# Kernel optimization log

Hardware: AMD Instinct MI355X
Metric: run time of the kernel (lower is better)

Reference implementation:

```python
import jax, jax.numpy as jnp
import numpy as np

T, B, E, H = 2048, 4, 768, 12
HD = E // H


def setup_inputs() -> dict:
    root = jax.random.key(0)
    ks = jax.random.split(root, 7)
    def xavier(k, shape):
        fan_in, fan_out = shape[1], shape[0]
        lim = (6.0 / (fan_in + fan_out)) ** 0.5
        return jax.random.uniform(k, shape, jnp.float32, -lim, lim)
    return {
        "query": jax.random.normal(ks[0], (T, B, E), jnp.float32),
        "key": jax.random.normal(ks[1], (T, B, E), jnp.float32),
        "value": jax.random.normal(ks[2], (T, B, E), jnp.float32),
        "in_proj_weight": xavier(ks[3], (3 * E, E)),
        "in_proj_bias": jnp.zeros((3 * E,), jnp.float32),
        "out_w": xavier(ks[4], (E, E)),
        "out_b": jnp.zeros((E,), jnp.float32),
    }


def reference(query, key, value, in_proj_weight, in_proj_bias, out_w, out_b):
    scaling = HD ** -0.5
    # separate Q/K/V projections from slices of the fused in_proj weight
    q = (query @ in_proj_weight[:E].T + in_proj_bias[:E]) * scaling
    k = key @ in_proj_weight[E:2 * E].T + in_proj_bias[E:2 * E]
    v = value @ in_proj_weight[2 * E:].T + in_proj_bias[2 * E:]
    tgt_len, bsz, _ = query.shape
    src_len = key.shape[0]
    # [T,B,E] -> [B,H,T,hd]
    qh = q.reshape(tgt_len, bsz, H, HD).transpose(1, 2, 0, 3)
    kh = k.reshape(src_len, bsz, H, HD).transpose(1, 2, 0, 3)
    vh = v.reshape(src_len, bsz, H, HD).transpose(1, 2, 0, 3)
    # full attention matrix [B,H,T,S] (faithful to the bmm-softmax-bmm impl)
    scores = jnp.einsum("bhqd,bhkd->bhqk", qh, kh)
    weights = jax.nn.softmax(scores, axis=-1)  # attn_dropout = 0.0 (eval)
    attn = jnp.einsum("bhqk,bhkd->bhqd", weights, vh)
    attn = attn.transpose(2, 0, 1, 3).reshape(tgt_len, bsz, E)
    out = attn @ out_w.T + out_b
    avg_weights = weights.sum(axis=1) / H  # [B,T,S]
    return out, avg_weights
```

## Files before the change

### kernel.cpp

```cpp
#include <hip/hip_runtime.h>

typedef unsigned short u16;
typedef unsigned long long u64;
typedef __attribute__((ext_vector_type(8))) short bf16x8;
typedef __attribute__((ext_vector_type(4))) float f32x4;
typedef __attribute__((ext_vector_type(16))) float f32x16;
typedef __attribute__((ext_vector_type(4))) _Float16 f16x4;
typedef __attribute__((ext_vector_type(2))) __fp16 h16x2;

#define TT 2048
#define BB 4
#define EE 768
#define HH 12
#define HD 64
#define NTOK 8192
#define KVB 32
#define NTILE (TT / KVB)

__device__ __forceinline__ u16 f2bf(float f) {
  unsigned int u = __builtin_bit_cast(unsigned int, f);
  u += 0x7fffu + ((u >> 16) & 1u);
  return (u16)(u >> 16);
}

__device__ __forceinline__ float bf2f(u16 b) {
  unsigned int u = (unsigned int)b << 16;
  return __builtin_bit_cast(float, u);
}

__device__ __forceinline__ unsigned int pack2(u16 a, u16 b) {
  return (unsigned int)a | ((unsigned int)b << 16);
}

__device__ __forceinline__ unsigned int cvtpk2(float a, float b) {
  unsigned int r;
  asm("v_cvt_pk_bf16_f32 %0, %1, %2" : "=v"(r) : "v"(a), "v"(b));
  return r;
}

__device__ __forceinline__ unsigned int pkh2(float a, float b) {
  h16x2 t = __builtin_amdgcn_cvt_pkrtz(a, b);
  return __builtin_bit_cast(unsigned int, t);
}

__global__ __launch_bounds__(256, 3) void proj_qkv(
    const float* __restrict__ q_in, const float* __restrict__ k_in, const float* __restrict__ v_in,
    const float* __restrict__ ipw, const float* __restrict__ ipb,
    u16* __restrict__ qh, u16* __restrict__ kh, u16* __restrict__ vh)
{
  __shared__ u16 sA[2][128 * 40];
  __shared__ u16 sB[2][192 * 40];
  const int tid = threadIdx.x;
  const int w = tid >> 6, lane = tid & 63, l32 = lane & 31, hi = lane >> 5;
  const int wm = w & 1, wn = w >> 1;
  const int orig = blockIdx.x;
  const int wg = (orig & 7) * 96 + (orig >> 3);
  const int z = wg >> 8;
  const int rem = wg & 255;
  const int bm = rem >> 2, bn = rem & 3;

  const float* A = (z == 0) ? q_in : (z == 1) ? k_in : v_in;
  const float* W = ipw + (size_t)z * EE * EE;
  const float* bias = ipb + z * EE;

  const int srow = tid >> 3, scs = tid & 7;
  const float* ag = A + (size_t)(bm * 128 + srow) * EE + scs * 4;
  const float* wgp = W + (size_t)(bn * 192 + srow) * EE + scs * 4;

  f32x16 acc[2][3] = {};
  float4 la[4], lw[6];

#pragma unroll
  for (int i = 0; i < 4; ++i) la[i] = *(const float4*)(ag + (size_t)i * 32 * EE);
#pragma unroll
  for (int i = 0; i < 6; ++i) lw[i] = *(const float4*)(wgp + (size_t)i * 32 * EE);
#pragma unroll
  for (int i = 0; i < 4; ++i) {
    u64 pk = (u64)cvtpk2(la[i].x, la[i].y) | ((u64)cvtpk2(la[i].z, la[i].w) << 32);
    *(u64*)&sA[0][(i * 32 + srow) * 40 + scs * 4] = pk;
  }
#pragma unroll
  for (int i = 0; i < 6; ++i) {
    u64 pk = (u64)cvtpk2(lw[i].x, lw[i].y) | ((u64)cvtpk2(lw[i].z, lw[i].w) << 32);
    *(u64*)&sB[0][(i * 32 + srow) * 40 + scs * 4] = pk;
  }

  for (int kt = 0; kt < EE / 32; ++kt) {
    const int buf = kt & 1;
    const bool more = (kt + 1) < EE / 32;
    if (more) {
      const int ko = (kt + 1) * 32;
#pragma unroll
      for (int i = 0; i < 4; ++i) la[i] = *(const float4*)(ag + (size_t)i * 32 * EE + ko);
#pragma unroll
      for (int i = 0; i < 6; ++i) lw[i] = *(const float4*)(wgp + (size_t)i * 32 * EE + ko);
    }
    __syncthreads();
#pragma unroll
    for (int ks = 0; ks < 2; ++ks) {
      bf16x8 bfr[3];
#pragma unroll
      for (int tn = 0; tn < 3; ++tn)
        bfr[tn] = *(const bf16x8*)&sB[buf][(wn * 96 + tn * 32 + l32) * 40 + ks * 16 + hi * 8];
#pragma unroll
      for (int tm = 0; tm < 2; ++tm) {
        bf16x8 afr = *(const bf16x8*)&sA[buf][(wm * 64 + tm * 32 + l32) * 40 + ks * 16 + hi * 8];
#pragma unroll
        for (int tn = 0; tn < 3; ++tn)
          acc[tm][tn] = __builtin_amdgcn_mfma_f32_32x32x16_bf16(afr, bfr[tn], acc[tm][tn], 0, 0, 0);
      }
    }
    if (more) {
      const int nb = buf ^ 1;
#pragma unroll
      for (int i = 0; i < 4; ++i) {
        u64 pk = (u64)cvtpk2(la[i].x, la[i].y) | ((u64)cvtpk2(la[i].z, la[i].w) << 32);
        *(u64*)&sA[nb][(i * 32 + srow) * 40 + scs * 4] = pk;
      }
#pragma unroll
      for (int i = 0; i < 6; ++i) {
        u64 pk = (u64)cvtpk2(lw[i].x, lw[i].y) | ((u64)cvtpk2(lw[i].z, lw[i].w) << 32);
        *(u64*)&sB[nb][(i * 32 + srow) * 40 + scs * 4] = pk;
      }
    }
  }

  const float scale = (z == 0) ? 0.125f : 1.0f;
  u16* dst = (z == 0) ? qh : (z == 1) ? kh : vh;
#pragma unroll
  for (int tn = 0; tn < 3; ++tn) {
    const int j = bn * 192 + wn * 96 + tn * 32 + l32;
    const int h = j >> 6, d = j & 63;
    const float bj = bias[j];
#pragma unroll
    for (int tm = 0; tm < 2; ++tm) {
#pragma unroll
      for (int r = 0; r < 16; ++r) {
        int m = bm * 128 + wm * 64 + tm * 32 + (r & 3) + 8 * (r >> 2) + 4 * hi;
        int t = m >> 2, bb = m & 3;
        float v = (acc[tm][tn][r] + bj) * scale;
        dst[((size_t)((bb * HH + h) * TT + t)) * HD + d] = f2bf(v);
      }
    }
  }
}

__global__ __launch_bounds__(256) void transpose_v(
    const u16* __restrict__ vh, _Float16* __restrict__ vhT)
{
  __shared__ u16 tile[64][72];
  const int tid = threadIdx.x;
  const int bh = blockIdx.y;
  const int t0 = blockIdx.x * 64;
  {
    int row = tid >> 2, seg = tid & 3;
    const u16* src = vh + (size_t)bh * TT * HD + (size_t)(t0 + row) * HD + seg * 16;
    uint4 a = *(const uint4*)(src);
    uint4 b = *(const uint4*)(src + 8);
    *(uint4*)&tile[row][seg * 16] = a;
    *(uint4*)&tile[row][seg * 16 + 8] = b;
  }
  __syncthreads();
  {
    int d = tid >> 2, ts = tid & 3;
    u16 tmp[16];
#pragma unroll
    for (int i = 0; i < 16; ++i) tmp[i] = tile[ts * 16 + i][d];
    unsigned int pk[8];
#pragma unroll
    for (int i = 0; i < 8; ++i)
      pk[i] = pkh2(bf2f(tmp[2 * i]), bf2f(tmp[2 * i + 1]));
    uint4 o0, o1;
    o0.x = pk[0]; o0.y = pk[1]; o0.z = pk[2]; o0.w = pk[3];
    o1.x = pk[4]; o1.y = pk[5]; o1.z = pk[6]; o1.w = pk[7];
    _Float16* dst = vhT + (size_t)bh * HD * TT + (size_t)d * TT + t0 + ts * 16;
    *(uint4*)dst = o0;
    *(uint4*)(dst + 8) = o1;
  }
}

__global__ __launch_bounds__(256, 3) void attn_flash(
    const u16* __restrict__ qh, const u16* __restrict__ kh, const _Float16* __restrict__ vhT,
    u16* __restrict__ ctx, float* __restrict__ stats_rl)
{
  __shared__ u16 sK[2][KVB * 64];
  __shared__ _Float16 sV[2][64 * 36];

  const int tid = threadIdx.x, w = tid >> 6, lane = tid & 63;
  const int l16 = lane & 15, quad = lane >> 4;
  const int orig = blockIdx.x;
  const int wg = (orig & 7) * 96 + (orig >> 3);
  const int qb = wg & 15;
  const int bhl = wg >> 4;
  const int b = bhl / HH, h = bhl - b * HH;
  const int q0 = qb * 128 + w * 32;
  const size_t bh = (size_t)bhl;
  const u16* qg = qh + (bh * TT + q0) * HD;
  const u16* kg = kh + bh * TT * HD;
  const _Float16* vg = vhT + bh * HD * TT;

  const int krow = tid >> 3, kch = tid & 7;
  const int kdst = krow * 64 + ((kch ^ (krow & 7)) * 8);
  const u16* kgp = kg + (size_t)krow * HD + kch * 8;
  const int vrow = tid >> 2, vch = tid & 3;
  const int vdst = vrow * 36 + vch * 8;
  const _Float16* vgp = vg + (size_t)vrow * TT + vch * 8;

  bf16x8 qf[2][2];
#pragma unroll
  for (int j = 0; j < 2; ++j)
#pragma unroll
    for (int p = 0; p < 2; ++p)
      qf[j][p] = *(const bf16x8*)(qg + (j * 16 + l16) * HD + p * 32 + quad * 8);

  f32x4 oacc[2][4] = {};
  float lsum[2] = {0.0f, 0.0f};

  {
    uint4 kv = *(const uint4*)kgp;
    uint4 vv = *(const uint4*)vgp;
    *(uint4*)&sK[0][kdst] = kv;
    *(u64*)&sV[0][vdst]     = ((const u64*)&vv)[0];
    *(u64*)&sV[0][vdst + 4] = ((const u64*)&vv)[1];
  }

  for (int st = 0; st < NTILE; ++st) {
    const int buf = st & 1;
    uint4 nk, nv;
    const bool more = (st + 1 < NTILE);
    if (more) {
      nk = *(const uint4*)(kgp + (size_t)(st + 1) * KVB * HD);
      nv = *(const uint4*)(vgp + (st + 1) * KVB);
    }
    __syncthreads();

    const u16* kb = &sK[buf][0];
    const _Float16* vb = &sV[buf][0];
#pragma unroll
    for (int ss = 0; ss < 2; ++ss) {
      const int krw = ss * 16 + l16;
      bf16x8 kf0 = *(const bf16x8*)&kb[krw * 64 + ((quad ^ (krw & 7)) * 8)];
      bf16x8 kf1 = *(const bf16x8*)&kb[krw * 64 + (((4 + quad) ^ (krw & 7)) * 8)];
      f16x4 vf[4];
#pragma unroll
      for (int m = 0; m < 4; ++m)
        vf[m] = *(const f16x4*)&vb[(m * 16 + l16) * 36 + ss * 16 + quad * 4];
#pragma unroll
      for (int j = 0; j < 2; ++j) {
        f32x4 z = {};
        f32x4 T = __builtin_amdgcn_mfma_f32_16x16x32_bf16(kf0, qf[j][0], z, 0, 0, 0);
        T = __builtin_amdgcn_mfma_f32_16x16x32_bf16(kf1, qf[j][1], T, 0, 0, 0);
        float p0 = __expf(T[0]), p1 = __expf(T[1]), p2 = __expf(T[2]), p3 = __expf(T[3]);
        lsum[j] += (p0 + p1) + (p2 + p3);
        uint2 uu;
        uu.x = pkh2(p0, p1);
        uu.y = pkh2(p2, p3);
        f16x4 pb = __builtin_bit_cast(f16x4, uu);
#pragma unroll
        for (int m = 0; m < 4; ++m)
          oacc[j][m] = __builtin_amdgcn_mfma_f32_16x16x16f16(vf[m], pb, oacc[j][m], 0, 0, 0);
      }
    }

    if (more) {
      const int nb = buf ^ 1;
      *(uint4*)&sK[nb][kdst] = nk;
      *(u64*)&sV[nb][vdst]     = ((const u64*)&nv)[0];
      *(u64*)&sV[nb][vdst + 4] = ((const u64*)&nv)[1];
    }
  }

#pragma unroll
  for (int j = 0; j < 2; ++j) {
    float s = lsum[j];
    s += __shfl_xor(s, 16);
    s += __shfl_xor(s, 32);
    float rl = 1.0f / s;
    const int q = q0 + j * 16 + l16;
    if (quad == 0) stats_rl[bh * TT + q] = rl;
    u16* crow = ctx + (size_t)(q * BB + b) * EE + h * HD;
#pragma unroll
    for (int m = 0; m < 4; ++m) {
      u64 pk =
          (u64)pack2(f2bf(oacc[j][m][0] * rl), f2bf(oacc[j][m][1] * rl)) |
          ((u64)pack2(f2bf(oacc[j][m][2] * rl), f2bf(oacc[j][m][3] * rl)) << 32);
      *(u64*)(crow + m * 16 + quad * 4) = pk;
    }
  }
}

__global__ __launch_bounds__(256) void attn_avg(
    const u16* __restrict__ qh, const u16* __restrict__ kh,
    const float* __restrict__ stats_rl, float* __restrict__ avg)
{
  const int tid = threadIdx.x, w = tid >> 6, lane = tid & 63;
  const int l16 = lane & 15, quad = lane >> 4;
  const int b = blockIdx.z;
  const int q0 = blockIdx.y * 128 + (w & 1) * 64;
  const int s0 = blockIdx.x * 128 + (w >> 1) * 64;

  f32x4 aacc[4][4] = {};

  for (int h = 0; h < HH; ++h) {
    const size_t bh = (size_t)(b * HH + h);
    const u16* qg = qh + (bh * TT + q0) * HD;
    const u16* kg = kh + (bh * TT + s0) * HD;

    bf16x8 qf[4][2], kf[4][2];
#pragma unroll
    for (int t = 0; t < 4; ++t)
#pragma unroll
      for (int ks = 0; ks < 2; ++ks) {
        qf[t][ks] = *(const bf16x8*)(qg + (t * 16 + l16) * HD + ks * 32 + quad * 8);
        kf[t][ks] = *(const bf16x8*)(kg + (t * 16 + l16) * HD + ks * 32 + quad * 8);
      }

    float4 lv[4];
#pragma unroll
    for (int tm = 0; tm < 4; ++tm)
      lv[tm] = *(const float4*)(stats_rl + bh * TT + q0 + tm * 16 + quad * 4);

#pragma unroll
    for (int nt = 0; nt < 4; ++nt) {
      f32x4 sacc[4] = {};
#pragma unroll
      for (int ks = 0; ks < 2; ++ks)
#pragma unroll
        for (int tm = 0; tm < 4; ++tm)
          sacc[tm] = __builtin_amdgcn_mfma_f32_16x16x32_bf16(qf[tm][ks], kf[nt][ks], sacc[tm], 0, 0, 0);
#pragma unroll
      for (int tm = 0; tm < 4; ++tm) {
        const float* rlp = (const float*)&lv[tm];
#pragma unroll
        for (int r = 0; r < 4; ++r)
          aacc[tm][nt][r] += __expf(sacc[tm][r]) * rlp[r];
      }
    }
  }

  const float ih = 1.0f / HH;
#pragma unroll
  for (int tm = 0; tm < 4; ++tm)
#pragma unroll
    for (int r = 0; r < 4; ++r) {
      int q = q0 + tm * 16 + quad * 4 + r;
#pragma unroll
      for (int nt = 0; nt < 4; ++nt)
        avg[((size_t)b * TT + q) * TT + s0 + nt * 16 + l16] = aacc[tm][nt][r] * ih;
    }
}

__global__ __launch_bounds__(256, 3) void proj_out(
    const u16* __restrict__ ctx, const float* __restrict__ ow, const float* __restrict__ ob,
    float* __restrict__ out)
{
  __shared__ u16 sA[2][128 * 40];
  __shared__ u16 sB[2][64 * 40];
  const int tid = threadIdx.x;
  const int w = tid >> 6, lane = tid & 63, l32 = lane & 31, hi = lane >> 5;
  const int wm = w & 1, wn = w >> 1;
  const int bn = blockIdx.x, bm = blockIdx.y;

  const int arow = tid >> 2, acs = tid & 3;
  const u16* ag = ctx + (size_t)(bm * 128 + arow) * EE + acs * 8;
  const int brow = tid >> 3, bcs = tid & 7;
  const float* wg2 = ow + (size_t)(bn * 64 + brow) * EE + bcs * 4;

  f32x16 acc[2] = {};
  uint4 lca[2]; float4 lwb[2];

#pragma unroll
  for (int i = 0; i < 2; ++i) lca[i] = *(const uint4*)(ag + (size_t)i * 64 * EE);
#pragma unroll
  for (int i = 0; i < 2; ++i) lwb[i] = *(const float4*)(wg2 + (size_t)i * 32 * EE);
#pragma unroll
  for (int i = 0; i < 2; ++i)
    *(uint4*)&sA[0][(i * 64 + arow) * 40 + acs * 8] = lca[i];
#pragma unroll
  for (int i = 0; i < 2; ++i) {
    u64 pk = (u64)cvtpk2(lwb[i].x, lwb[i].y) | ((u64)cvtpk2(lwb[i].z, lwb[i].w) << 32);
    *(u64*)&sB[0][(i * 32 + brow) * 40 + bcs * 4] = pk;
  }

  for (int kt = 0; kt < EE / 32; ++kt) {
    const int buf = kt & 1;
    const bool more = (kt + 1) < EE / 32;
    if (more) {
      const int ko = (kt + 1) * 32;
#pragma unroll
      for (int i = 0; i < 2; ++i) lca[i] = *(const uint4*)(ag + (size_t)i * 64 * EE + ko);
#pragma unroll
      for (int i = 0; i < 2; ++i) lwb[i] = *(const float4*)(wg2 + (size_t)i * 32 * EE + ko);
    }
    __syncthreads();
#pragma unroll
    for (int ks = 0; ks < 2; ++ks) {
      bf16x8 bfr = *(const bf16x8*)&sB[buf][(wn * 32 + l32) * 40 + ks * 16 + hi * 8];
#pragma unroll
      for (int tm = 0; tm < 2; ++tm) {
        bf16x8 afr = *(const bf16x8*)&sA[buf][(wm * 64 + tm * 32 + l32) * 40 + ks * 16 + hi * 8];
        acc[tm] = __builtin_amdgcn_mfma_f32_32x32x16_bf16(afr, bfr, acc[tm], 0, 0, 0);
      }
    }
    if (more) {
      const int nb = buf ^ 1;
#pragma unroll
      for (int i = 0; i < 2; ++i)
        *(uint4*)&sA[nb][(i * 64 + arow) * 40 + acs * 8] = lca[i];
#pragma unroll
      for (int i = 0; i < 2; ++i) {
        u64 pk = (u64)cvtpk2(lwb[i].x, lwb[i].y) | ((u64)cvtpk2(lwb[i].z, lwb[i].w) << 32);
        *(u64*)&sB[nb][(i * 32 + brow) * 40 + bcs * 4] = pk;
      }
    }
  }

  const int j = bn * 64 + wn * 32 + l32;
  const float bj = ob[j];
#pragma unroll
  for (int tm = 0; tm < 2; ++tm) {
#pragma unroll
    for (int r = 0; r < 16; ++r) {
      int m = bm * 128 + wm * 64 + tm * 32 + (r & 3) + 8 * (r >> 2) + 4 * hi;
      out[(size_t)m * EE + j] = acc[tm][r] + bj;
    }
  }
}

extern "C" void kernel_launch(void* const* d_in, const int* in_sizes, int n_in,
                              void* d_out, int out_size, void* d_ws, size_t ws_size,
                              hipStream_t stream)
{
  const float* query = (const float*)d_in[0];
  const float* key   = (const float*)d_in[1];
  const float* value = (const float*)d_in[2];
  const float* ipw   = (const float*)d_in[3];
  const float* ipb   = (const float*)d_in[4];
  const float* ow    = (const float*)d_in[5];
  const float* ob    = (const float*)d_in[6];
  float* out = (float*)d_out;

  char* p = (char*)d_ws;
  const size_t QKV = (size_t)BB * HH * TT * HD * 2;
  u16* qh  = (u16*)p; p += QKV;
  u16* kh  = (u16*)p; p += QKV;
  u16* vh  = (u16*)p; p += QKV;
  _Float16* vhT = (_Float16*)p; p += QKV;
  u16* ctx = (u16*)p; p += (size_t)NTOK * EE * 2;
  float* stats = (float*)p;

  proj_qkv<<<dim3(768, 1, 1), 256, 0, stream>>>(query, key, value, ipw, ipb, qh, kh, vh);
  transpose_v<<<dim3(32, 48), 256, 0, stream>>>(vh, vhT);
  attn_flash<<<dim3(768, 1, 1), 256, 0, stream>>>(qh, kh, vhT, ctx, stats);
  attn_avg<<<dim3(16, 16, BB), 256, 0, stream>>>(qh, kh, stats, out + (size_t)NTOK * EE);
  proj_out<<<dim3(12, 64), 256, 0, stream>>>(ctx, ow, ob, out);
}
```

Measured before the change: 421.8 us.

## Stage Q/K tiles in swizzled LDS with register prefetch in attn_avg

The attn_avg kernel now loads the 128x64 Q and K tiles for each head cooperatively into XOR-swizzled shared memory, and prefetches the next head's tiles into registers while the current head computes. Previously each wave read its fragments straight from global memory. The MFMA operands are swapped (K times Q) so each lane holds four consecutive key columns, which allows float4 coalesced stores of the large averaged-weights output instead of scalar strided stores. The change adds two barriers per head and 32KB of LDS, which may reduce occupancy.

```diff
diff --git a/kernel.cpp b/kernel.cpp
--- a/kernel.cpp
+++ b/kernel.cpp
@@ -293,61 +293,105 @@
     const u16* __restrict__ qh, const u16* __restrict__ kh,
     const float* __restrict__ stats_rl, float* __restrict__ avg)
 {
+  __shared__ u16 sQ[128 * 64];
+  __shared__ u16 sK[128 * 64];
   const int tid = threadIdx.x, w = tid >> 6, lane = tid & 63;
   const int l16 = lane & 15, quad = lane >> 4;
   const int b = blockIdx.z;
-  const int q0 = blockIdx.y * 128 + (w & 1) * 64;
-  const int s0 = blockIdx.x * 128 + (w >> 1) * 64;
+  const int q0 = blockIdx.y * 128, s0 = blockIdx.x * 128;
+  const int wq = (w & 1) * 64, ws = (w >> 1) * 64;
+
+  const int srow = tid >> 3, sch = tid & 7;
+  const int sdst = (sch ^ (srow & 7)) * 8;
 
   f32x4 aacc[4][4] = {};
+  uint4 stq[4], stk[4];
+
+  {
+    const size_t bh0 = (size_t)b * HH;
+    const u16* qg = qh + (bh0 * TT + q0 + srow) * HD + sch * 8;
+    const u16* kg = kh + (bh0 * TT + s0 + srow) * HD + sch * 8;
+#pragma unroll
+    for (int i = 0; i < 4; ++i) {
+      stq[i] = *(const uint4*)(qg + (size_t)i * 32 * HD);
+      stk[i] = *(const uint4*)(kg + (size_t)i * 32 * HD);
+    }
+  }
+#pragma unroll
+  for (int i = 0; i < 4; ++i) {
+    *(uint4*)&sQ[(i * 32 + srow) * 64 + sdst] = stq[i];
+    *(uint4*)&sK[(i * 32 + srow) * 64 + sdst] = stk[i];
+  }
 
   for (int h = 0; h < HH; ++h) {
     const size_t bh = (size_t)(b * HH + h);
-    const u16* qg = qh + (bh * TT + q0) * HD;
-    const u16* kg = kh + (bh * TT + s0) * HD;
-
-    bf16x8 qf[4][2], kf[4][2];
+    __syncthreads();
+
+    const bool more = (h + 1) < HH;
+    if (more) {
+      const u16* qg = qh + ((bh + 1) * TT + q0 + srow) * HD + sch * 8;
+      const u16* kg = kh + ((bh + 1) * TT + s0 + srow) * HD + sch * 8;
+#pragma unroll
+      for (int i = 0; i < 4; ++i) {
+        stq[i] = *(const uint4*)(qg + (size_t)i * 32 * HD);
+        stk[i] = *(const uint4*)(kg + (size_t)i * 32 * HD);
+      }
+    }
+
+    bf16x8 qf[4][2];
 #pragma unroll
     for (int t = 0; t < 4; ++t)
 #pragma unroll
       for (int ks = 0; ks < 2; ++ks) {
-        qf[t][ks] = *(const bf16x8*)(qg + (t * 16 + l16) * HD + ks * 32 + quad * 8);
-        kf[t][ks] = *(const bf16x8*)(kg + (t * 16 + l16) * HD + ks * 32 + quad * 8);
-      }
-
-    float4 lv[4];
-#pragma unroll
-    for (int tm = 0; tm < 4; ++tm)
-      lv[tm] = *(const float4*)(stats_rl + bh * TT + q0 + tm * 16 + quad * 4);
+        const int row = wq + t * 16 + l16;
+        qf[t][ks] = *(const bf16x8*)&sQ[row * 64 + (((ks * 4 + quad) ^ (row & 7)) * 8)];
+      }
+    float rlv[4];
+#pragma unroll
+    for (int t = 0; t < 4; ++t)
+      rlv[t] = stats_rl[bh * TT + q0 + wq + t * 16 + l16];
 
 #pragma unroll
     for (int nt = 0; nt < 4; ++nt) {
-      f32x4 sacc[4] = {};
-#pragma unroll
-      for (int ks = 0; ks < 2; ++ks)
-#pragma unroll
-        for (int tm = 0; tm < 4; ++tm)
-          sacc[tm] = __builtin_amdgcn_mfma_f32_16x16x32_bf16(qf[tm][ks], kf[nt][ks], sacc[tm], 0, 0, 0);
+      const int krow = ws + nt * 16 + l16;
+      bf16x8 kf0 = *(const bf16x8*)&sK[krow * 64 + ((quad ^ (krow & 7)) * 8)];
+      bf16x8 kf1 = *(const bf16x8*)&sK[krow * 64 + (((4 + quad) ^ (krow & 7)) * 8)];
 #pragma unroll
       for (int tm = 0; tm < 4; ++tm) {
-        const float* rlp = (const float*)&lv[tm];
+        f32x4 sacc = {};
+        sacc = __builtin_amdgcn_mfma_f32_16x16x32_bf16(kf0, qf[tm][0], sacc, 0, 0, 0);
+        sacc = __builtin_amdgcn_mfma_f32_16x16x32_bf16(kf1, qf[tm][1], sacc, 0, 0, 0);
 #pragma unroll
         for (int r = 0; r < 4; ++r)
-          aacc[tm][nt][r] += __expf(sacc[tm][r]) * rlp[r];
+          aacc[tm][nt][r] += __expf(sacc[r]) * rlv[tm];
+      }
+    }
+
+    __syncthreads();
+    if (more) {
+#pragma unroll
+      for (int i = 0; i < 4; ++i) {
+        *(uint4*)&sQ[(i * 32 + srow) * 64 + sdst] = stq[i];
+        *(uint4*)&sK[(i * 32 + srow) * 64 + sdst] = stk[i];
       }
     }
   }
 
   const float ih = 1.0f / HH;
 #pragma unroll
-  for (int tm = 0; tm < 4; ++tm)
-#pragma unroll
-    for (int r = 0; r < 4; ++r) {
-      int q = q0 + tm * 16 + quad * 4 + r;
-#pragma unroll
-      for (int nt = 0; nt < 4; ++nt)
-        avg[((size_t)b * TT + q) * TT + s0 + nt * 16 + l16] = aacc[tm][nt][r] * ih;
-    }
+  for (int tm = 0; tm < 4; ++tm) {
+    const int q = q0 + wq + tm * 16 + l16;
+    float* orow = avg + ((size_t)b * TT + q) * TT + s0 + ws;
+#pragma unroll
+    for (int nt = 0; nt < 4; ++nt) {
+      float4 o;
+      o.x = aacc[tm][nt][0] * ih;
+      o.y = aacc[tm][nt][1] * ih;
+      o.z = aacc[tm][nt][2] * ih;
+      o.w = aacc[tm][nt][3] * ih;
+      *(float4*)(orow + nt * 16 + quad * 4) = o;
+    }
+  }
 }
 
 __global__ __launch_bounds__(256, 3) void proj_out(
```

After: 473.0 us. 12.2% more time.
